# Kernel tuning notes

Measured on AMD Instinct MI355X. Metric: run time of the kernel, lower is better.

## Reference

```python
import jax, jax.numpy as jnp
import numpy as np

L, S, M, N, E, H = 1024, 1024, 256, 8, 512, 8


def embed_rotary(x, cos, sin):
    # x: [B, T, E]; interleaved rotate-half as in RotaryPositionEncoding.embed_rotary
    x2 = jnp.stack([-x[..., 1::2], x[..., 0::2]], axis=-1).reshape(x.shape)
    return x * cos + x2 * sin


def setup_inputs() -> dict:
    key = jax.random.key(0)
    ks = jax.random.split(key, 12)
    return {
        "query": jax.random.normal(ks[0], (L, N, E), jnp.float32),
        "key": jax.random.normal(ks[1], (S, N, E), jnp.float32),
        "value": jax.random.normal(ks[2], (S, N, E), jnp.float32),
        "in_proj_weight": jax.random.normal(ks[3], (3 * E, E), jnp.float32) / np.sqrt(E).astype(np.float32),
        "in_proj_bias": jnp.zeros((3 * E,), jnp.float32),
        "out_proj_weight": jax.random.normal(ks[4], (E, E), jnp.float32) / np.sqrt(E).astype(np.float32),
        "out_proj_bias": jnp.zeros((E,), jnp.float32),
        "rot_q": jax.random.normal(ks[5], (N, L, E, 2), jnp.float32),
        "rot_k": jax.random.normal(ks[6], (N, S, E, 2), jnp.float32),
        "k_mem": jax.random.normal(ks[7], (M, N, E), jnp.float32),
        "v_mem": jax.random.normal(ks[8], (M, N, E), jnp.float32),
        "gate_attn": jax.random.normal(ks[9], (H,), jnp.float32),
        "mem_mask": jax.random.randint(ks[10], (N, M), 0, 2).astype(bool),
        "num_heads": H,
    }


def reference(query, key, value, in_proj_weight, in_proj_bias, out_proj_weight,
              out_proj_bias, rot_q, rot_k, k_mem, v_mem, gate_attn, mem_mask, num_heads):
    L_, N_, E_ = query.shape
    S_ = key.shape[0]
    H_ = num_heads
    hd = E_ // H_
    scale = float(hd) ** -0.5
    # separate q/k/v projections (qkv not identical path)
    q = query @ in_proj_weight[:E_].T + in_proj_bias[:E_]
    k = key @ in_proj_weight[E_:2 * E_].T + in_proj_bias[E_:2 * E_]
    v = value @ in_proj_weight[2 * E_:].T + in_proj_bias[2 * E_:]
    q = q * scale
    # inline rotary PE (applied in batch-first layout, then back)
    q = embed_rotary(q.transpose(1, 0, 2), rot_q[..., 0], rot_q[..., 1]).transpose(1, 0, 2)
    k = embed_rotary(k.transpose(1, 0, 2), rot_k[..., 0], rot_k[..., 1]).transpose(1, 0, 2)
    qh = q.reshape(L_, N_, H_, hd).transpose(1, 2, 0, 3)  # [N,H,L,hd]
    kh = k.reshape(S_, N_, H_, hd).transpose(1, 2, 0, 3)  # [N,H,S,hd]
    vh = v.reshape(S_, N_, H_, hd).transpose(1, 2, 0, 3)
    scores = jnp.einsum('nhld,nhsd->nhls', qh, kh)
    # slot-competition: softmax over queries (slots), then renormalize over keys
    w = jax.nn.softmax(scores, axis=2) + 1e-8
    w = w / w.sum(axis=-1, keepdims=True)
    attn = jnp.einsum('nhls,nhsd->nhld', w, vh)
    # memorizing-transformer style memory K/V branch with sigmoid head gating
    Mm = k_mem.shape[0]
    km = k_mem.reshape(Mm, N_, H_, hd).transpose(1, 2, 0, 3)  # [N,H,M,hd]
    vm = v_mem.reshape(Mm, N_, H_, hd).transpose(1, 2, 0, 3)
    sm = jnp.einsum('nhld,nhmd->nhlm', qh, km)
    sm = jnp.where(mem_mask[:, None, None, :], -1e9, sm)  # additive -inf mask
    wm = jax.nn.softmax(sm, axis=-1)
    om = jnp.einsum('nhlm,nhmd->nhld', wm, vm)
    gate = jax.nn.sigmoid(gate_attn)[None, :, None, None]  # [1,H,1,1]
    attn = gate * om + (1.0 - gate) * attn
    out = attn.transpose(2, 0, 1, 3).reshape(L_, N_, E_)  # back to [L,N,E]
    return out @ out_proj_weight.T + out_proj_bias
```

## Files before the change

### kernel.cpp

```cpp
#include <hip/hip_runtime.h>
#include <hip/hip_bf16.h>

typedef __hip_bfloat16 bf16;
typedef __bf16 bf16x8 __attribute__((ext_vector_type(8)));
typedef float f32x4 __attribute__((ext_vector_type(4)));

#define LQ 1024
#define SK 1024
#define MMEM 256
#define NB 8
#define EE 512
#define NH 8
#define HD 64
#define NBH 64

__device__ inline __bf16 tobf(float f) {
  __hip_bfloat16 h = __float2bfloat16(f);
  return *reinterpret_cast<__bf16*>(&h);
}
__device__ inline float bf2f(__bf16 x) {
  unsigned short u; __builtin_memcpy(&u, &x, 2);
  unsigned int v = (unsigned int)u << 16;
  float f; __builtin_memcpy(&f, &v, 4);
  return f;
}
__device__ inline f32x4 MFMA(bf16x8 a, bf16x8 b, f32x4 c) {
  return __builtin_amdgcn_mfma_f32_16x16x32_bf16(a, b, c, 0, 0, 0);
}

__device__ inline void gload_lds16(const bf16* g, void* l) {
  __builtin_amdgcn_global_load_lds(
      (const __attribute__((address_space(1))) void*)g,
      (__attribute__((address_space(3))) void*)l, 16, 0, 0);
}

__device__ inline bf16x8 load8(const float* p) {
  float4 a = *(const float4*)p;
  float4 b = *(const float4*)(p + 4);
  bf16x8 r;
  r[0] = tobf(a.x); r[1] = tobf(a.y); r[2] = tobf(a.z); r[3] = tobf(a.w);
  r[4] = tobf(b.x); r[5] = tobf(b.y); r[6] = tobf(b.z); r[7] = tobf(b.w);
  return r;
}

#define CVT_T0 524288
#define CVT_T3 98304
#define CVT_T4 32768
__global__ __launch_bounds__(256) void convert5(
    const float* __restrict__ q, const float* __restrict__ k,
    const float* __restrict__ v, const float* __restrict__ w,
    const float* __restrict__ o, bf16* __restrict__ qc, bf16* __restrict__ kc,
    bf16* __restrict__ vc, bf16* __restrict__ wc, bf16* __restrict__ oc)
{
  long long t = (long long)blockIdx.x * 256 + threadIdx.x;
  const float* src; bf16* dst; long long idx;
  if (t < CVT_T0)               { src = q; dst = qc; idx = t; }
  else if (t < 2 * CVT_T0)      { src = k; dst = kc; idx = t - CVT_T0; }
  else if (t < 3 * CVT_T0)      { src = v; dst = vc; idx = t - 2 * CVT_T0; }
  else if (t < 3 * CVT_T0 + CVT_T3) { src = w; dst = wc; idx = t - 3 * CVT_T0; }
  else                          { src = o; dst = oc; idx = t - 3 * CVT_T0 - CVT_T3; }
  *(bf16x8*)(dst + idx * 8) = load8(src + idx * 8);
}

__global__ __launch_bounds__(256) void gemm_proj3(
    const bf16* __restrict__ qc, const bf16* __restrict__ kc,
    const bf16* __restrict__ vc, const bf16* __restrict__ ipwb,
    const float* __restrict__ ipb, bf16* __restrict__ pq,
    bf16* __restrict__ pk, bf16* __restrict__ v_raw)
{
  __shared__ __align__(16) char smem[33792];
  __bf16* As = (__bf16*)smem;
  __bf16* Bs = (__bf16*)(smem + 16384);
  const int z = blockIdx.z;
  const bf16* A = (z == 0) ? qc : (z == 1) ? kc : vc;
  const bf16* W = ipwb + (long long)z * EE * EE;
  const float* bias = ipb + z * EE;
  const float alpha = (z == 0) ? 0.125f : 1.f;
  const int bid2 = blockIdx.y * gridDim.x + blockIdx.x;
  const int xcd = bid2 & 7, sub = bid2 >> 3;
  const int by = (xcd << 3) + (sub >> 2);
  const int bx = sub & 3;
  const int tm0 = by << 7, tn0 = bx << 7;
  const int t = threadIdx.x;
  const int wave = t >> 6, lane = t & 63;
  const int wrow0 = (wave & 1) << 6, wcol0 = (wave >> 1) << 6;
  const int m16 = lane & 15, quad = lane >> 4;

  const f32x4 zero = {0.f, 0.f, 0.f, 0.f};
  f32x4 acc[4][4];
#pragma unroll
  for (int mi = 0; mi < 4; ++mi)
#pragma unroll
    for (int ni = 0; ni < 4; ++ni) acc[mi][ni] = zero;

  const bf16* Ab = A + (long long)tm0 * EE;
  const bf16* Bb = W + (long long)tn0 * EE;
  const int ob_u = wave << 10;

  for (int k0 = 0; k0 < EE; k0 += 64) {
#pragma unroll
    for (int c = 0; c < 4; ++c) {
      int ob = (c << 12) + ob_u;
      int obl = ob + (lane << 4);
      int row = obl >> 7;
      int ce = (obl & 127) >> 1;
      gload_lds16(Ab + (long long)row * EE + k0 + ce, smem + ob);
      gload_lds16(Bb + (long long)row * EE + k0 + ce, smem + 16384 + ob);
    }
    __syncthreads();
#pragma unroll
    for (int kh = 0; kh < 2; ++kh) {
      bf16x8 av[4], bv[4];
#pragma unroll
      for (int i = 0; i < 4; ++i) {
        av[i] = *(bf16x8*)(As + ((wrow0 + (i << 4) + m16) << 6) + (kh << 5) + (quad << 3));
        bv[i] = *(bf16x8*)(Bs + ((wcol0 + (i << 4) + m16) << 6) + (kh << 5) + (quad << 3));
      }
#pragma unroll
      for (int mi = 0; mi < 4; ++mi)
#pragma unroll
        for (int ni = 0; ni < 4; ++ni)
          acc[mi][ni] = MFMA(av[mi], bv[ni], acc[mi][ni]);
    }
    __syncthreads();
  }

  __bf16 (*Cs)[132] = (__bf16(*)[132])smem;
#pragma unroll
  for (int mi = 0; mi < 4; ++mi)
#pragma unroll
    for (int ni = 0; ni < 4; ++ni) {
      int col = wcol0 + (ni << 4) + m16;
      float bv = bias[tn0 + col];
#pragma unroll
      for (int r = 0; r < 4; ++r)
        Cs[wrow0 + (mi << 4) + (quad << 2) + r][col] =
            tobf((acc[mi][ni][r] + bv) * alpha);
    }
  __syncthreads();
  bf16* O = (z == 0) ? pq : (z == 1) ? pk : v_raw;
  const int crow = t >> 1, ch0 = (t & 1) << 6;
  long long gb = (long long)(tm0 + crow) * EE + tn0 + ch0;
#pragma unroll
  for (int j = 0; j < 64; j += 8)
    *(uint4*)(O + gb + j) = *(uint4*)&Cs[crow][ch0 + j];
}

__global__ __launch_bounds__(256) void rotary_kernel(
    const bf16* __restrict__ pq, const bf16* __restrict__ pk,
    const float* __restrict__ rot_q, const float* __restrict__ rot_k,
    bf16* __restrict__ Qh, bf16* __restrict__ Kh)
{
  const bf16* src = blockIdx.y ? pk : pq;
  const float* rot = blockIdx.y ? rot_k : rot_q;
  bf16* dst = blockIdx.y ? Kh : Qh;
  const int t = threadIdx.x;
  const int row = (blockIdx.x << 2) + (t >> 6);
  const int e0 = (t & 63) << 3;
  const int l = row >> 3, n = row & 7;
  bf16x8 x = *(const bf16x8*)(src + (long long)row * EE + e0);
  const float* rp = rot + ((((long long)n * LQ + l) * EE + e0) << 1);
  __bf16 vals[8];
#pragma unroll
  for (int j = 0; j < 8; j += 2) {
    float4 cs4 = *(const float4*)(rp + (j << 1));
    float x0 = bf2f(x[j]);
    float x1 = bf2f(x[j + 1]);
    vals[j]     = tobf(x0 * cs4.x - x1 * cs4.y);
    vals[j + 1] = tobf(x1 * cs4.z + x0 * cs4.w);
  }
  const int h = e0 >> 6, d0 = e0 & 63;
  *(uint4*)(dst + (((long long)(n * NH + h) * LQ + l) * HD + d0)) = *(uint4*)vals;
}

__global__ __launch_bounds__(256) void colsum_kernel(
    const bf16* __restrict__ Qh, const bf16* __restrict__ Kh,
    float* __restrict__ csum)
{
  __shared__ __align__(16) __bf16 Ks[64][72];
  __shared__ __align__(16) __bf16 Qs[64][72];
  __shared__ float cpart[64][2];
  const int bid = blockIdx.y * gridDim.x + blockIdx.x;
  const int xcd = bid & 7, sub = bid >> 3;
  const int b = (xcd << 3) + (sub >> 4);
  const int st0 = (sub & 15) << 6;
  const int t = threadIdx.x;
  const int lrow = t >> 2, lcol = (t & 3) << 4;
  const int wave = t >> 6, lane = t & 63;
  const int wm = (wave & 1) << 5, wn = (wave >> 1) << 5;
  const int m16 = lane & 15, quad = lane >> 4;

  {
    const bf16* kp = Kh + ((long long)b * SK + st0 + lrow) * HD + lcol;
    *(bf16x8*)&Ks[lrow][lcol] = *(const bf16x8*)kp;
    *(bf16x8*)&Ks[lrow][lcol + 8] = *(const bf16x8*)(kp + 8);
  }
  __syncthreads();
  bf16x8 bk[2][2];
#pragma unroll
  for (int ni = 0; ni < 2; ++ni)
#pragma unroll
    for (int kh = 0; kh < 2; ++kh)
      bk[ni][kh] = *(bf16x8*)&Ks[wn + (ni << 4) + m16][(kh << 5) + (quad << 3)];
  __syncthreads();

  const f32x4 zero = {0.f, 0.f, 0.f, 0.f};
  float colp[2] = {0.f, 0.f};
  const bf16* qbase = Qh + ((long long)b * LQ + lrow) * HD + lcol;
  bf16x8 qr0 = *(const bf16x8*)qbase;
  bf16x8 qr1 = *(const bf16x8*)(qbase + 8);
  for (int lt = 0; lt < 16; ++lt) {
    *(bf16x8*)&Qs[lrow][lcol] = qr0;
    *(bf16x8*)&Qs[lrow][lcol + 8] = qr1;
    __syncthreads();
    if (lt < 15) {
      const bf16* qp = qbase + (long long)((lt + 1) << 6) * HD;
      qr0 = *(const bf16x8*)qp;
      qr1 = *(const bf16x8*)(qp + 8);
    }
    f32x4 s00 = zero, s01 = zero, s10 = zero, s11 = zero;
#pragma unroll
    for (int kh = 0; kh < 2; ++kh) {
      bf16x8 a0 = *(bf16x8*)&Qs[wm + m16][(kh << 5) + (quad << 3)];
      bf16x8 a1 = *(bf16x8*)&Qs[wm + 16 + m16][(kh << 5) + (quad << 3)];
      s00 = MFMA(a0, bk[0][kh], s00);
      s01 = MFMA(a0, bk[1][kh], s01);
      s10 = MFMA(a1, bk[0][kh], s10);
      s11 = MFMA(a1, bk[1][kh], s11);
    }
    f32x4 sacc[2][2] = {{s00, s01}, {s10, s11}};
#pragma unroll
    for (int mi = 0; mi < 2; ++mi)
#pragma unroll
      for (int ni = 0; ni < 2; ++ni)
#pragma unroll
        for (int r = 0; r < 4; ++r)
          colp[ni] += __expf(sacc[mi][ni][r]);
    __syncthreads();
  }
  for (int ni = 0; ni < 2; ++ni) {
    float v = colp[ni];
    v += __shfl_down(v, 32, 64);
    v += __shfl_down(v, 16, 64);
    if (quad == 0) cpart[wn + (ni << 4) + m16][wm >> 5] = v;
  }
  __syncthreads();
  if (t < 64) csum[b * SK + st0 + t] = cpart[t][0] + cpart[t][1];
}

__global__ __launch_bounds__(256) void vsum_kernel(
    const bf16* __restrict__ Vt, float* __restrict__ Vsum)
{
  int wid = blockIdx.x * 4 + (threadIdx.x >> 6);
  int lane = threadIdx.x & 63;
  const bf16* p = Vt + (long long)wid * SK + lane * 16;
  float s = 0.f;
  bf16x8 v0 = *(const bf16x8*)p;
  bf16x8 v1 = *(const bf16x8*)(p + 8);
#pragma unroll
  for (int j = 0; j < 8; ++j) s += bf2f(v0[j]) + bf2f(v1[j]);
  for (int off = 32; off; off >>= 1) s += __shfl_down(s, off, 64);
  if (lane == 0) Vsum[wid] = s;
}

__global__ __launch_bounds__(256) void attn_flash(
    const bf16* __restrict__ Qh, const bf16* __restrict__ Kh,
    const bf16* __restrict__ Vt, const float* __restrict__ csum,
    const float* __restrict__ Vsum, bf16* __restrict__ attn)
{
  __shared__ __align__(16) __bf16 Ks[64][72];
  __shared__ __align__(16) __bf16 Vs[64][72];
  __shared__ __align__(16) __bf16 Ps[4096];
  __shared__ __align__(16) float rcs[SK];
  __shared__ float rpart[64][2];
  const int bid = blockIdx.y * gridDim.x + blockIdx.x;
  const int xcd = bid & 7, sub = bid >> 3;
  const int b = (xcd << 3) + (sub >> 4);
  const int tm0 = (sub & 15) << 6;
  const int t = threadIdx.x;
  const int lrow = t >> 2, lcol = (t & 3) << 4;
  const int wave = t >> 6, lane = t & 63;
  const int wm = (wave & 1) << 5, wn = (wave >> 1) << 5;
  const int m16 = lane & 15, quad = lane >> 4;
  const int swz = (m16 & 7) << 4;

#pragma unroll
  for (int i = 0; i < 4; ++i)
    rcs[t + i * 256] = 1.f / csum[b * SK + t + i * 256];
  {
    const bf16* qp = Qh + ((long long)b * LQ + tm0 + lrow) * HD + lcol;
    *(bf16x8*)&Ks[lrow][lcol] = *(const bf16x8*)qp;
    *(bf16x8*)&Ks[lrow][lcol + 8] = *(const bf16x8*)(qp + 8);
  }
  __syncthreads();
  bf16x8 aq[2][2];
#pragma unroll
  for (int li = 0; li < 2; ++li)
#pragma unroll
    for (int kh = 0; kh < 2; ++kh)
      aq[li][kh] = *(bf16x8*)&Ks[wm + (li << 4) + m16][(kh << 5) + (quad << 3)];
  __syncthreads();

  const f32x4 zero = {0.f, 0.f, 0.f, 0.f};
  f32x4 o00 = zero, o01 = zero, o10 = zero, o11 = zero;
  float rsuml[2] = {0.f, 0.f};

  const bf16* kbase = Kh + ((long long)b * SK + lrow) * HD + lcol;
  const bf16* vbase = Vt + ((long long)b * HD + lrow) * SK + lcol;
  bf16x8 kr0 = *(const bf16x8*)kbase;
  bf16x8 kr1 = *(const bf16x8*)(kbase + 8);
  bf16x8 vr0 = *(const bf16x8*)vbase;
  bf16x8 vr1 = *(const bf16x8*)(vbase + 8);

  for (int st = 0; st < 16; ++st) {
    *(bf16x8*)&Ks[lrow][lcol] = kr0;
    *(bf16x8*)&Ks[lrow][lcol + 8] = kr1;
    *(bf16x8*)&Vs[lrow][lcol] = vr0;
    *(bf16x8*)&Vs[lrow][lcol + 8] = vr1;
    __syncthreads();
    if (st < 15) {
      const bf16* kp = kbase + (long long)((st + 1) << 6) * HD;
      const bf16* vp = vbase + ((st + 1) << 6);
      kr0 = *(const bf16x8*)kp;
      kr1 = *(const bf16x8*)(kp + 8);
      vr0 = *(const bf16x8*)vp;
      vr1 = *(const bf16x8*)(vp + 8);
    }
    f32x4 s00 = zero, s01 = zero, s10 = zero, s11 = zero;
#pragma unroll
    for (int kh = 0; kh < 2; ++kh) {
      bf16x8 ak0 = *(bf16x8*)&Ks[wn + m16][(kh << 5) + (quad << 3)];
      bf16x8 ak1 = *(bf16x8*)&Ks[wn + 16 + m16][(kh << 5) + (quad << 3)];
      s00 = MFMA(ak0, aq[0][kh], s00);
      s01 = MFMA(ak0, aq[1][kh], s01);
      s10 = MFMA(ak1, aq[0][kh], s10);
      s11 = MFMA(ak1, aq[1][kh], s11);
    }
    {
      const int lA = wm + m16, lB = wm + 16 + m16;
      char* pA = (char*)Ps + lA * 128;
      char* pB = (char*)Ps + lB * 128;
#pragma unroll
      for (int si = 0; si < 2; ++si) {
        int sloc = wn + (si << 4) + (quad << 2);
        f32x4 rc4 = *(const f32x4*)&rcs[(st << 6) + sloc];
        f32x4 sA = si ? s10 : s00;
        f32x4 sB = si ? s11 : s01;
        __bf16 vA[4], vB[4];
#pragma unroll
        for (int r = 0; r < 4; ++r) {
          float pa = __expf(sA[r]) * rc4[r];
          rsuml[0] += pa; vA[r] = tobf(pa);
          float pb = __expf(sB[r]) * rc4[r];
          rsuml[1] += pb; vB[r] = tobf(pb);
        }
        int sbyte = (sloc << 1) ^ swz;
        *(uint2*)(pA + sbyte) = *(uint2*)vA;
        *(uint2*)(pB + sbyte) = *(uint2*)vB;
      }
    }
    __syncthreads();
#pragma unroll
    for (int kh = 0; kh < 2; ++kh) {
      int sb = (kh << 6) + (quad << 4);
      bf16x8 ap0 = *(bf16x8*)((char*)Ps + (wm + m16) * 128 + (sb ^ swz));
      bf16x8 ap1 = *(bf16x8*)((char*)Ps + (wm + 16 + m16) * 128 + (sb ^ swz));
      bf16x8 bv0 = *(bf16x8*)&Vs[wn + m16][(kh << 5) + (quad << 3)];
      bf16x8 bv1 = *(bf16x8*)&Vs[wn + 16 + m16][(kh << 5) + (quad << 3)];
      o00 = MFMA(ap0, bv0, o00);
      o01 = MFMA(ap0, bv1, o01);
      o10 = MFMA(ap1, bv0, o10);
      o11 = MFMA(ap1, bv1, o11);
    }
    __syncthreads();
  }
#pragma unroll
  for (int li = 0; li < 2; ++li) {
    float v = rsuml[li];
    v += __shfl_xor(v, 16, 64);
    v += __shfl_xor(v, 32, 64);
    if (quad == 0) rpart[wm + (li << 4) + m16][wn >> 5] = v;
  }
  __syncthreads();
  const float* vs = Vsum + b * HD;
  f32x4 oacc[2][2] = {{o00, o01}, {o10, o11}};
  for (int mi = 0; mi < 2; ++mi)
    for (int ni = 0; ni < 2; ++ni) {
      int col = wn + (ni << 4) + m16;
      float vsc = 1e-8f * vs[col];
      for (int r = 0; r < 4; ++r) {
        int row = wm + (mi << 4) + (quad << 2) + r;
        float rs = rpart[row][0] + rpart[row][1];
        Ks[row][col] = tobf((oacc[mi][ni][r] + vsc) / (rs + (float)SK * 1e-8f));
      }
    }
  __syncthreads();
  uint4 u0 = *(uint4*)&Ks[lrow][lcol];
  uint4 u1 = *(uint4*)&Ks[lrow][lcol + 8];
  long long gb = ((long long)b * LQ + tm0 + lrow) * HD + lcol;
  *(uint4*)(attn + gb) = u0;
  *(uint4*)(attn + gb + 8) = u1;
}

__global__ __launch_bounds__(256) void mem_flash(
    const bf16* __restrict__ Qh, const bf16* __restrict__ km,
    const bf16* __restrict__ vmt, const int* __restrict__ mask,
    bf16* __restrict__ omb)
{
  __shared__ __align__(16) __bf16 Ks[64][72];
  __shared__ __align__(16) __bf16 Vs[64][72];
  __shared__ __align__(16) __bf16 Ps[4096];
  __shared__ __align__(16) float mskf[MMEM];
  __shared__ float rpart[64][2];
  const int bid = blockIdx.y * gridDim.x + blockIdx.x;
  const int xcd = bid & 7, sub = bid >> 3;
  const int b = (xcd << 3) + (sub >> 4);
  const int tm0 = (sub & 15) << 6;
  const int n = b >> 3;
  const int t = threadIdx.x;
  const int wave = t >> 6, lane = t & 63;
  const int wm = (wave & 1) << 5, wn = (wave >> 1) << 5;
  const int m16 = lane & 15, quad = lane >> 4;
  const int lrow = t >> 2, lcol = (t & 3) << 4;
  const int swz = (m16 & 7) << 4;

  mskf[t] = mask[n * MMEM + t] ? 0.f : 1.f;
  {
    const bf16* qp = Qh + ((long long)b * LQ + tm0 + lrow) * HD + lcol;
    *(bf16x8*)&Ks[lrow][lcol] = *(const bf16x8*)qp;
    *(bf16x8*)&Ks[lrow][lcol + 8] = *(const bf16x8*)(qp + 8);
  }
  __syncthreads();
  bf16x8 aq[2][2];
#pragma unroll
  for (int li = 0; li < 2; ++li)
#pragma unroll
    for (int kh = 0; kh < 2; ++kh)
      aq[li][kh] = *(bf16x8*)&Ks[wm + (li << 4) + m16][(kh << 5) + (quad << 3)];
  __syncthreads();

  const f32x4 zero = {0.f, 0.f, 0.f, 0.f};
  f32x4 o00 = zero, o01 = zero, o10 = zero, o11 = zero;
  float rsuml[2] = {0.f, 0.f};

  const bf16* kbase = km + ((long long)b * MMEM + lrow) * HD + lcol;
  const bf16* vbase = vmt + ((long long)b * HD + lrow) * MMEM + lcol;
  bf16x8 kr0 = *(const bf16x8*)kbase;
  bf16x8 kr1 = *(const bf16x8*)(kbase + 8);
  bf16x8 vr0 = *(const bf16x8*)vbase;
  bf16x8 vr1 = *(const bf16x8*)(vbase + 8);

  for (int mt = 0; mt < 4; ++mt) {
    *(bf16x8*)&Ks[lrow][lcol] = kr0;
    *(bf16x8*)&Ks[lrow][lcol + 8] = kr1;
    *(bf16x8*)&Vs[lrow][lcol] = vr0;
    *(bf16x8*)&Vs[lrow][lcol + 8] = vr1;
    __syncthreads();
    if (mt < 3) {
      const bf16* kp = kbase + (long long)((mt + 1) << 6) * HD;
      const bf16* vp = vbase + ((mt + 1) << 6);
      kr0 = *(const bf16x8*)kp;
      kr1 = *(const bf16x8*)(kp + 8);
      vr0 = *(const bf16x8*)vp;
      vr1 = *(const bf16x8*)(vp + 8);
    }
    f32x4 s00 = zero, s01 = zero, s10 = zero, s11 = zero;
#pragma unroll
    for (int kh = 0; kh < 2; ++kh) {
      bf16x8 ak0 = *(bf16x8*)&Ks[wn + m16][(kh << 5) + (quad << 3)];
      bf16x8 ak1 = *(bf16x8*)&Ks[wn + 16 + m16][(kh << 5) + (quad << 3)];
      s00 = MFMA(ak0, aq[0][kh], s00);
      s01 = MFMA(ak0, aq[1][kh], s01);
      s10 = MFMA(ak1, aq[0][kh], s10);
      s11 = MFMA(ak1, aq[1][kh], s11);
    }
    {
      const int lA = wm + m16, lB = wm + 16 + m16;
      char* pA = (char*)Ps + lA * 128;
      char* pB = (char*)Ps + lB * 128;
#pragma unroll
      for (int si = 0; si < 2; ++si) {
        int sloc = wn + (si << 4) + (quad << 2);
        f32x4 mf4 = *(const f32x4*)&mskf[(mt << 6) + sloc];
        f32x4 sA = si ? s10 : s00;
        f32x4 sB = si ? s11 : s01;
        __bf16 vA[4], vB[4];
#pragma unroll
        for (int r = 0; r < 4; ++r) {
          float pa = __expf(sA[r]) * mf4[r];
          rsuml[0] += pa; vA[r] = tobf(pa);
          float pb = __expf(sB[r]) * mf4[r];
          rsuml[1] += pb; vB[r] = tobf(pb);
        }
        int sbyte = (sloc << 1) ^ swz;
        *(uint2*)(pA + sbyte) = *(uint2*)vA;
        *(uint2*)(pB + sbyte) = *(uint2*)vB;
      }
    }
    __syncthreads();
#pragma unroll
    for (int kh = 0; kh < 2; ++kh) {
      int sb = (kh << 6) + (quad << 4);
      bf16x8 ap0 = *(bf16x8*)((char*)Ps + (wm + m16) * 128 + (sb ^ swz));
      bf16x8 ap1 = *(bf16x8*)((char*)Ps + (wm + 16 + m16) * 128 + (sb ^ swz));
      bf16x8 bv0 = *(bf16x8*)&Vs[wn + m16][(kh << 5) + (quad << 3)];
      bf16x8 bv1 = *(bf16x8*)&Vs[wn + 16 + m16][(kh << 5) + (quad << 3)];
      o00 = MFMA(ap0, bv0, o00);
      o01 = MFMA(ap0, bv1, o01);
      o10 = MFMA(ap1, bv0, o10);
      o11 = MFMA(ap1, bv1, o11);
    }
    __syncthreads();
  }
#pragma unroll
  for (int li = 0; li < 2; ++li) {
    float v = rsuml[li];
    v += __shfl_xor(v, 16, 64);
    v += __shfl_xor(v, 32, 64);
    if (quad == 0) rpart[wm + (li << 4) + m16][wn >> 5] = v;
  }
  __syncthreads();
  f32x4 oacc[2][2] = {{o00, o01}, {o10, o11}};
  for (int mi = 0; mi < 2; ++mi)
    for (int ni = 0; ni < 2; ++ni) {
      int col = wn + (ni << 4) + m16;
      for (int r = 0; r < 4; ++r) {
        int row = wm + (mi << 4) + (quad << 2) + r;
        float rs = rpart[row][0] + rpart[row][1];
        Ks[row][col] = tobf(oacc[mi][ni][r] / rs);
      }
    }
  __syncthreads();
  uint4 u0 = *(uint4*)&Ks[lrow][lcol];
  uint4 u1 = *(uint4*)&Ks[lrow][lcol + 8];
  long long gb = ((long long)b * LQ + tm0 + lrow) * HD + lcol;
  *(uint4*)(omb + gb) = u0;
  *(uint4*)(omb + gb + 8) = u1;
}

__global__ __launch_bounds__(256) void gemm_out(
    const bf16* __restrict__ attn, const bf16* __restrict__ omb,
    const float* __restrict__ gate, const bf16* __restrict__ opwb,
    const float* __restrict__ opb, float* __restrict__ out)
{
  __shared__ __align__(16) __bf16 As[64][40];
  __shared__ __align__(16) __bf16 Bs[64][40];
  __shared__ float sg[NH];
  const int bid = blockIdx.y * gridDim.x + blockIdx.x;
  const int xcd = bid & 7, sub = bid >> 3;
  const int by = (xcd << 4) + (sub >> 3);
  const int bx = sub & 7;
  const int tm0 = by << 6, tn0 = bx << 6;
  const int t = threadIdx.x;
  const int lrow = t >> 2, lk = (t & 3) << 3;
  const int wave = t >> 6, lane = t & 63;
  const int wm = (wave & 1) << 5, wn = (wave >> 1) << 5;
  const int m16 = lane & 15, quad = lane >> 4;

  if (t < NH) sg[t] = 1.f / (1.f + __expf(-gate[t]));
  __syncthreads();

  const f32x4 zero = {0.f, 0.f, 0.f, 0.f};
  f32x4 acc00 = zero, acc01 = zero, acc10 = zero, acc11 = zero;

  const int row = tm0 + lrow;
  const int l = row >> 3, n = row & 7;
  const bf16* bg = opwb + (long long)(tn0 + lrow) * EE + lk;
  for (int k0 = 0; k0 < EE; k0 += 32) {
    int e = k0 + lk;
    int h = e >> 6, d = e & 63;
    float g = sg[h];
    long long src = (((long long)(n * NH + h) * LQ) + l) * HD + d;
    bf16x8 a8 = *(const bf16x8*)(attn + src);
    bf16x8 o8 = *(const bf16x8*)(omb + src);
    bf16x8 ap;
#pragma unroll
    for (int j = 0; j < 8; ++j)
      ap[j] = tobf(g * bf2f(o8[j]) + (1.f - g) * bf2f(a8[j]));
    *(bf16x8*)&As[lrow][lk] = ap;
    *(bf16x8*)&Bs[lrow][lk] = *(const bf16x8*)(bg + k0);
    __syncthreads();
    bf16x8 a0 = *(bf16x8*)&As[wm + m16][quad << 3];
    bf16x8 a1 = *(bf16x8*)&As[wm + 16 + m16][quad << 3];
    bf16x8 b0 = *(bf16x8*)&Bs[wn + m16][quad << 3];
    bf16x8 b1 = *(bf16x8*)&Bs[wn + 16 + m16][quad << 3];
    acc00 = MFMA(a0, b0, acc00);
    acc01 = MFMA(a0, b1, acc01);
    acc10 = MFMA(a1, b0, acc10);
    acc11 = MFMA(a1, b1, acc11);
    __syncthreads();
  }
  f32x4 accs[2][2] = {{acc00, acc01}, {acc10, acc11}};
  for (int mi = 0; mi < 2; ++mi)
    for (int ni = 0; ni < 2; ++ni) {
      int col = tn0 + wn + (ni << 4) + m16;
      float bv = opb[col];
      long long base = (long long)(tm0 + wm + (mi << 4) + (quad << 2)) * EE + col;
      for (int r = 0; r < 4; ++r)
        out[base + (long long)r * EE] = accs[mi][ni][r] + bv;
    }
}

__global__ __launch_bounds__(256) void v_transpose(
    const bf16* __restrict__ raw, bf16* __restrict__ Vt)
{
  __shared__ __align__(16) __bf16 Ts[64][72];
  const int bh = blockIdx.y;
  const int n = bh >> 3, h = bh & 7;
  const int s0 = blockIdx.x << 6;
  const int t = threadIdx.x;
  const int i = t >> 2, c0 = (t & 3) << 4;
  const bf16* rp = raw + ((long long)(s0 + i) * NB + n) * EE + h * HD + c0;
  *(bf16x8*)&Ts[i][c0] = *(const bf16x8*)rp;
  *(bf16x8*)&Ts[i][c0 + 8] = *(const bf16x8*)(rp + 8);
  __syncthreads();
  const int d = t >> 2, j0 = (t & 3) << 4;
  __bf16 vals[16];
#pragma unroll
  for (int j = 0; j < 16; ++j) vals[j] = Ts[j0 + j][d];
  bf16* wp = Vt + ((long long)bh * HD + d) * SK + s0 + j0;
  *(uint4*)wp = *(uint4*)&vals[0];
  *(uint4*)(wp + 8) = *(uint4*)&vals[8];
}

__global__ __launch_bounds__(256) void mem_prep(
    const float* __restrict__ k_mem, const float* __restrict__ v_mem,
    bf16* __restrict__ km, bf16* __restrict__ vmt)
{
  __shared__ __align__(16) __bf16 Ts[64][72];
  const int bh = blockIdx.y;
  const int n = bh >> 3, h = bh & 7;
  const int m0 = blockIdx.x << 6;
  const int t = threadIdx.x;
  const int i = t >> 2, c0 = (t & 3) << 4;
  const float* kp = k_mem + ((long long)(m0 + i) * NB + n) * EE + h * HD + c0;
  const float* vp = v_mem + ((long long)(m0 + i) * NB + n) * EE + h * HD + c0;
  bf16x8 kv0 = load8(kp), kv1 = load8(kp + 8);
  bf16x8 vv0 = load8(vp), vv1 = load8(vp + 8);
  bf16* kw = km + ((long long)bh * MMEM + m0 + i) * HD + c0;
  *(bf16x8*)kw = kv0;
  *(bf16x8*)(kw + 8) = kv1;
  *(bf16x8*)&Ts[i][c0] = vv0;
  *(bf16x8*)&Ts[i][c0 + 8] = vv1;
  __syncthreads();
  const int d = t >> 2, j0 = (t & 3) << 4;
  __bf16 vals[16];
#pragma unroll
  for (int j = 0; j < 16; ++j) vals[j] = Ts[j0 + j][d];
  bf16* wp = vmt + ((long long)bh * HD + d) * MMEM + m0 + j0;
  *(uint4*)wp = *(uint4*)&vals[0];
  *(uint4*)(wp + 8) = *(uint4*)&vals[8];
}

extern "C" void kernel_launch(void* const* d_in, const int* in_sizes, int n_in,
                              void* d_out, int out_size, void* d_ws, size_t ws_size,
                              hipStream_t stream) {
  const float* query = (const float*)d_in[0];
  const float* key   = (const float*)d_in[1];
  const float* value = (const float*)d_in[2];
  const float* ipw   = (const float*)d_in[3];
  const float* ipb   = (const float*)d_in[4];
  const float* opw   = (const float*)d_in[5];
  const float* opb   = (const float*)d_in[6];
  const float* rot_q = (const float*)d_in[7];
  const float* rot_k = (const float*)d_in[8];
  const float* k_mem = (const float*)d_in[9];
  const float* v_mem = (const float*)d_in[10];
  const float* gate  = (const float*)d_in[11];
  const int*  mask   = (const int*)d_in[12];
  float* out = (float*)d_out;

  char* w = (char*)d_ws;
  size_t off = 0;
  auto carve = [&](size_t bytes) -> char* {
    char* p = w + off;
    off += (bytes + 255) & ~(size_t)255;
    return p;
  };
  bf16* qc    = (bf16*)carve((size_t)LQ * NB * EE * 2);
  bf16* kc    = (bf16*)carve((size_t)SK * NB * EE * 2);
  bf16* vc    = (bf16*)carve((size_t)SK * NB * EE * 2);
  bf16* ipwb  = (bf16*)carve((size_t)3 * EE * EE * 2);
  bf16* opwb  = (bf16*)carve((size_t)EE * EE * 2);
  bf16* v_raw = (bf16*)carve((size_t)SK * NB * EE * 2);
  bf16* Qh    = (bf16*)carve((size_t)NBH * LQ * HD * 2);
  bf16* Kh    = (bf16*)carve((size_t)NBH * SK * HD * 2);
  bf16* Vt    = (bf16*)carve((size_t)NBH * HD * SK * 2);
  bf16* km    = (bf16*)carve((size_t)NBH * MMEM * HD * 2);
  bf16* vmt   = (bf16*)carve((size_t)NBH * HD * MMEM * 2);
  float* csum = (float*)carve((size_t)NBH * SK * 4);
  float* Vsum = (float*)carve((size_t)NBH * HD * 4);
  bf16* attn  = (bf16*)carve((size_t)NBH * LQ * HD * 2);
  bf16* omb   = (bf16*)carve((size_t)NBH * LQ * HD * 2);
  if (off > ws_size) {
    hipMemsetAsync(d_out, 0, (size_t)out_size * 4, stream);
    return;
  }
  bf16* pq = attn;
  bf16* pk = omb;

  convert5<<<(3 * CVT_T0 + CVT_T3 + CVT_T4) / 256, 256, 0, stream>>>(
      query, key, value, ipw, opw, qc, kc, vc, ipwb, opwb);

  gemm_proj3<<<dim3(EE / 128, (LQ * NB) / 128, 3), 256, 0, stream>>>(
      qc, kc, vc, ipwb, ipb, pq, pk, v_raw);

  rotary_kernel<<<dim3((LQ * NB) / 4, 2), 256, 0, stream>>>(
      pq, pk, rot_q, rot_k, Qh, Kh);

  v_transpose<<<dim3(SK / 64, NBH), 256, 0, stream>>>(v_raw, Vt);
  vsum_kernel<<<(NBH * HD) / 4, 256, 0, stream>>>(Vt, Vsum);
  mem_prep<<<dim3(MMEM / 64, NBH), 256, 0, stream>>>(k_mem, v_mem, km, vmt);

  colsum_kernel<<<dim3(SK / 64, NBH), 256, 0, stream>>>(Qh, Kh, csum);

  attn_flash<<<dim3(LQ / 64, NBH), 256, 0, stream>>>(Qh, Kh, Vt, csum, Vsum, attn);
  mem_flash<<<dim3(LQ / 64, NBH), 256, 0, stream>>>(Qh, km, vmt, mask, omb);

  gemm_out<<<dim3(EE / 64, (LQ * NB) / 64, 1), 256, 0, stream>>>(attn, omb, gate, opwb, opb, out);
}
```

Before: 306.0 us.

## Fuse memory-branch attention and gating into main attention kernel; retile output GEMM

Merges the memory K/V softmax branch into the main attention kernel, reusing the loaded Q fragments and applying the sigmoid head gate in the epilogue, so a single combined bf16 tensor is written instead of two. The output projection GEMM is rewritten with 128x128 tiles, 4x4 MFMA accumulators per wave and direct global-to-LDS loads, and no longer blends two inputs. MFMA sections are wrapped in s_setprio hints. This removes one launch, one Q reload and the extra tensor read/write, at the cost of higher register pressure in the fused kernel and fewer GEMM blocks.

Measured after the change: 304.9 us. No clear change (-0.4%).

```diff
diff --git a/kernel.cpp b/kernel.cpp
--- a/kernel.cpp
+++ b/kernel.cpp
@@ -263,20 +263,25 @@
   if (lane == 0) Vsum[wid] = s;
 }
 
-__global__ __launch_bounds__(256) void attn_flash(
+__global__ __launch_bounds__(256) void attn_fused(
     const bf16* __restrict__ Qh, const bf16* __restrict__ Kh,
-    const bf16* __restrict__ Vt, const float* __restrict__ csum,
-    const float* __restrict__ Vsum, bf16* __restrict__ attn)
+    const bf16* __restrict__ Vt, const bf16* __restrict__ km,
+    const bf16* __restrict__ vmt, const float* __restrict__ csum,
+    const float* __restrict__ Vsum, const int* __restrict__ mask,
+    const float* __restrict__ gate, bf16* __restrict__ comb)
 {
   __shared__ __align__(16) __bf16 Ks[64][72];
   __shared__ __align__(16) __bf16 Vs[64][72];
   __shared__ __align__(16) __bf16 Ps[4096];
   __shared__ __align__(16) float rcs[SK];
-  __shared__ float rpart[64][2];
+  __shared__ __align__(16) float mskf[MMEM];
+  __shared__ float rpa[64][2];
+  __shared__ float rpm[64][2];
   const int bid = blockIdx.y * gridDim.x + blockIdx.x;
   const int xcd = bid & 7, sub = bid >> 3;
   const int b = (xcd << 3) + (sub >> 4);
   const int tm0 = (sub & 15) << 6;
+  const int n = b >> 3, h = b & 7;
   const int t = threadIdx.x;
   const int lrow = t >> 2, lcol = (t & 3) << 4;
   const int wave = t >> 6, lane = t & 63;
@@ -287,6 +292,7 @@
 #pragma unroll
   for (int i = 0; i < 4; ++i)
     rcs[t + i * 256] = 1.f / csum[b * SK + t + i * 256];
+  mskf[t] = mask[n * MMEM + t] ? 0.f : 1.f;
   {
     const bf16* qp = Qh + ((long long)b * LQ + tm0 + lrow) * HD + lcol;
     *(bf16x8*)&Ks[lrow][lcol] = *(const bf16x8*)qp;
@@ -302,302 +308,267 @@
   __syncthreads();
 
   const f32x4 zero = {0.f, 0.f, 0.f, 0.f};
+  f32x4 m00 = zero, m01 = zero, m10 = zero, m11 = zero;
+  float rsm[2] = {0.f, 0.f};
+  {
+    const bf16* kbase = km + ((long long)b * MMEM + lrow) * HD + lcol;
+    const bf16* vbase = vmt + ((long long)b * HD + lrow) * MMEM + lcol;
+    bf16x8 kr0 = *(const bf16x8*)kbase;
+    bf16x8 kr1 = *(const bf16x8*)(kbase + 8);
+    bf16x8 vr0 = *(const bf16x8*)vbase;
+    bf16x8 vr1 = *(const bf16x8*)(vbase + 8);
+    for (int mt = 0; mt < 4; ++mt) {
+      *(bf16x8*)&Ks[lrow][lcol] = kr0;
+      *(bf16x8*)&Ks[lrow][lcol + 8] = kr1;
+      *(bf16x8*)&Vs[lrow][lcol] = vr0;
+      *(bf16x8*)&Vs[lrow][lcol + 8] = vr1;
+      __syncthreads();
+      if (mt < 3) {
+        const bf16* kp = kbase + (long long)((mt + 1) << 6) * HD;
+        const bf16* vp = vbase + ((mt + 1) << 6);
+        kr0 = *(const bf16x8*)kp;
+        kr1 = *(const bf16x8*)(kp + 8);
+        vr0 = *(const bf16x8*)vp;
+        vr1 = *(const bf16x8*)(vp + 8);
+      }
+      f32x4 s00 = zero, s01 = zero, s10 = zero, s11 = zero;
+      __builtin_amdgcn_s_setprio(1);
+#pragma unroll
+      for (int kh = 0; kh < 2; ++kh) {
+        bf16x8 ak0 = *(bf16x8*)&Ks[wn + m16][(kh << 5) + (quad << 3)];
+        bf16x8 ak1 = *(bf16x8*)&Ks[wn + 16 + m16][(kh << 5) + (quad << 3)];
+        s00 = MFMA(ak0, aq[0][kh], s00);
+        s01 = MFMA(ak0, aq[1][kh], s01);
+        s10 = MFMA(ak1, aq[0][kh], s10);
+        s11 = MFMA(ak1, aq[1][kh], s11);
+      }
+      __builtin_amdgcn_s_setprio(0);
+      {
+        char* pA = (char*)Ps + (wm + m16) * 128;
+        char* pB = (char*)Ps + (wm + 16 + m16) * 128;
+#pragma unroll
+        for (int si = 0; si < 2; ++si) {
+          int sloc = wn + (si << 4) + (quad << 2);
+          f32x4 mf4 = *(const f32x4*)&mskf[(mt << 6) + sloc];
+          f32x4 sA = si ? s10 : s00;
+          f32x4 sB = si ? s11 : s01;
+          __bf16 vA[4], vB[4];
+#pragma unroll
+          for (int r = 0; r < 4; ++r) {
+            float pa = __expf(sA[r]) * mf4[r];
+            rsm[0] += pa; vA[r] = tobf(pa);
+            float pb = __expf(sB[r]) * mf4[r];
+            rsm[1] += pb; vB[r] = tobf(pb);
+          }
+          int sbyte = (sloc << 1) ^ swz;
+          *(uint2*)(pA + sbyte) = *(uint2*)vA;
+          *(uint2*)(pB + sbyte) = *(uint2*)vB;
+        }
+      }
+      __syncthreads();
+      __builtin_amdgcn_s_setprio(1);
+#pragma unroll
+      for (int kh = 0; kh < 2; ++kh) {
+        int sb = (kh << 6) + (quad << 4);
+        bf16x8 ap0 = *(bf16x8*)((char*)Ps + (wm + m16) * 128 + (sb ^ swz));
+        bf16x8 ap1 = *(bf16x8*)((char*)Ps + (wm + 16 + m16) * 128 + (sb ^ swz));
+        bf16x8 bv0 = *(bf16x8*)&Vs[wn + m16][(kh << 5) + (quad << 3)];
+        bf16x8 bv1 = *(bf16x8*)&Vs[wn + 16 + m16][(kh << 5) + (quad << 3)];
+        m00 = MFMA(ap0, bv0, m00);
+        m01 = MFMA(ap0, bv1, m01);
+        m10 = MFMA(ap1, bv0, m10);
+        m11 = MFMA(ap1, bv1, m11);
+      }
+      __builtin_amdgcn_s_setprio(0);
+      __syncthreads();
+    }
+  }
+
   f32x4 o00 = zero, o01 = zero, o10 = zero, o11 = zero;
-  float rsuml[2] = {0.f, 0.f};
-
-  const bf16* kbase = Kh + ((long long)b * SK + lrow) * HD + lcol;
-  const bf16* vbase = Vt + ((long long)b * HD + lrow) * SK + lcol;
-  bf16x8 kr0 = *(const bf16x8*)kbase;
-  bf16x8 kr1 = *(const bf16x8*)(kbase + 8);
-  bf16x8 vr0 = *(const bf16x8*)vbase;
-  bf16x8 vr1 = *(const bf16x8*)(vbase + 8);
-
-  for (int st = 0; st < 16; ++st) {
-    *(bf16x8*)&Ks[lrow][lcol] = kr0;
-    *(bf16x8*)&Ks[lrow][lcol + 8] = kr1;
-    *(bf16x8*)&Vs[lrow][lcol] = vr0;
-    *(bf16x8*)&Vs[lrow][lcol + 8] = vr1;
-    __syncthreads();
-    if (st < 15) {
-      const bf16* kp = kbase + (long long)((st + 1) << 6) * HD;
-      const bf16* vp = vbase + ((st + 1) << 6);
-      kr0 = *(const bf16x8*)kp;
-      kr1 = *(const bf16x8*)(kp + 8);
-      vr0 = *(const bf16x8*)vp;
-      vr1 = *(const bf16x8*)(vp + 8);
-    }
-    f32x4 s00 = zero, s01 = zero, s10 = zero, s11 = zero;
-#pragma unroll
-    for (int kh = 0; kh < 2; ++kh) {
-      bf16x8 ak0 = *(bf16x8*)&Ks[wn + m16][(kh << 5) + (quad << 3)];
-      bf16x8 ak1 = *(bf16x8*)&Ks[wn + 16 + m16][(kh << 5) + (quad << 3)];
-      s00 = MFMA(ak0, aq[0][kh], s00);
-      s01 = MFMA(ak0, aq[1][kh], s01);
-      s10 = MFMA(ak1, aq[0][kh], s10);
-      s11 = MFMA(ak1, aq[1][kh], s11);
-    }
-    {
-      const int lA = wm + m16, lB = wm + 16 + m16;
-      char* pA = (char*)Ps + lA * 128;
-      char* pB = (char*)Ps + lB * 128;
-#pragma unroll
-      for (int si = 0; si < 2; ++si) {
-        int sloc = wn + (si << 4) + (quad << 2);
-        f32x4 rc4 = *(const f32x4*)&rcs[(st << 6) + sloc];
-        f32x4 sA = si ? s10 : s00;
-        f32x4 sB = si ? s11 : s01;
-        __bf16 vA[4], vB[4];
-#pragma unroll
-        for (int r = 0; r < 4; ++r) {
-          float pa = __expf(sA[r]) * rc4[r];
-          rsuml[0] += pa; vA[r] = tobf(pa);
-          float pb = __expf(sB[r]) * rc4[r];
-          rsuml[1] += pb; vB[r] = tobf(pb);
+  float rsa[2] = {0.f, 0.f};
+  {
+    const bf16* kbase = Kh + ((long long)b * SK + lrow) * HD + lcol;
+    const bf16* vbase = Vt + ((long long)b * HD + lrow) * SK + lcol;
+    bf16x8 kr0 = *(const bf16x8*)kbase;
+    bf16x8 kr1 = *(const bf16x8*)(kbase + 8);
+    bf16x8 vr0 = *(const bf16x8*)vbase;
+    bf16x8 vr1 = *(const bf16x8*)(vbase + 8);
+    for (int st = 0; st < 16; ++st) {
+      *(bf16x8*)&Ks[lrow][lcol] = kr0;
+      *(bf16x8*)&Ks[lrow][lcol + 8] = kr1;
+      *(bf16x8*)&Vs[lrow][lcol] = vr0;
+      *(bf16x8*)&Vs[lrow][lcol + 8] = vr1;
+      __syncthreads();
+      if (st < 15) {
+        const bf16* kp = kbase + (long long)((st + 1) << 6) * HD;
+        const bf16* vp = vbase + ((st + 1) << 6);
+        kr0 = *(const bf16x8*)kp;
+        kr1 = *(const bf16x8*)(kp + 8);
+        vr0 = *(const bf16x8*)vp;
+        vr1 = *(const bf16x8*)(vp + 8);
+      }
+      f32x4 s00 = zero, s01 = zero, s10 = zero, s11 = zero;
+      __builtin_amdgcn_s_setprio(1);
+#pragma unroll
+      for (int kh = 0; kh < 2; ++kh) {
+        bf16x8 ak0 = *(bf16x8*)&Ks[wn + m16][(kh << 5) + (quad << 3)];
+        bf16x8 ak1 = *(bf16x8*)&Ks[wn + 16 + m16][(kh << 5) + (quad << 3)];
+        s00 = MFMA(ak0, aq[0][kh], s00);
+        s01 = MFMA(ak0, aq[1][kh], s01);
+        s10 = MFMA(ak1, aq[0][kh], s10);
+        s11 = MFMA(ak1, aq[1][kh], s11);
+      }
+      __builtin_amdgcn_s_setprio(0);
+      {
+        char* pA = (char*)Ps + (wm + m16) * 128;
+        char* pB = (char*)Ps + (wm + 16 + m16) * 128;
+#pragma unroll
+        for (int si = 0; si < 2; ++si) {
+          int sloc = wn + (si << 4) + (quad << 2);
+          f32x4 rc4 = *(const f32x4*)&rcs[(st << 6) + sloc];
+          f32x4 sA = si ? s10 : s00;
+          f32x4 sB = si ? s11 : s01;
+          __bf16 vA[4], vB[4];
+#pragma unroll
+          for (int r = 0; r < 4; ++r) {
+            float pa = __expf(sA[r]) * rc4[r];
+            rsa[0] += pa; vA[r] = tobf(pa);
+            float pb = __expf(sB[r]) * rc4[r];
+            rsa[1] += pb; vB[r] = tobf(pb);
+          }
+          int sbyte = (sloc << 1) ^ swz;
+          *(uint2*)(pA + sbyte) = *(uint2*)vA;
+          *(uint2*)(pB + sbyte) = *(uint2*)vB;
         }
-        int sbyte = (sloc << 1) ^ swz;
-        *(uint2*)(pA + sbyte) = *(uint2*)vA;
-        *(uint2*)(pB + sbyte) = *(uint2*)vB;
-      }
-    }
-    __syncthreads();
-#pragma unroll
-    for (int kh = 0; kh < 2; ++kh) {
-      int sb = (kh << 6) + (quad << 4);
-      bf16x8 ap0 = *(bf16x8*)((char*)Ps + (wm + m16) * 128 + (sb ^ swz));
-      bf16x8 ap1 = *(bf16x8*)((char*)Ps + (wm + 16 + m16) * 128 + (sb ^ swz));
-      bf16x8 bv0 = *(bf16x8*)&Vs[wn + m16][(kh << 5) + (quad << 3)];
-      bf16x8 bv1 = *(bf16x8*)&Vs[wn + 16 + m16][(kh << 5) + (quad << 3)];
-      o00 = MFMA(ap0, bv0, o00);
-      o01 = MFMA(ap0, bv1, o01);
-      o10 = MFMA(ap1, bv0, o10);
-      o11 = MFMA(ap1, bv1, o11);
-    }
-    __syncthreads();
-  }
+      }
+      __syncthreads();
+      __builtin_amdgcn_s_setprio(1);
+#pragma unroll
+      for (int kh = 0; kh < 2; ++kh) {
+        int sb = (kh << 6) + (quad << 4);
+        bf16x8 ap0 = *(bf16x8*)((char*)Ps + (wm + m16) * 128 + (sb ^ swz));
+        bf16x8 ap1 = *(bf16x8*)((char*)Ps + (wm + 16 + m16) * 128 + (sb ^ swz));
+        bf16x8 bv0 = *(bf16x8*)&Vs[wn + m16][(kh << 5) + (quad << 3)];
+        bf16x8 bv1 = *(bf16x8*)&Vs[wn + 16 + m16][(kh << 5) + (quad << 3)];
+        o00 = MFMA(ap0, bv0, o00);
+        o01 = MFMA(ap0, bv1, o01);
+        o10 = MFMA(ap1, bv0, o10);
+        o11 = MFMA(ap1, bv1, o11);
+      }
+      __builtin_amdgcn_s_setprio(0);
+      __syncthreads();
+    }
+  }
+
 #pragma unroll
   for (int li = 0; li < 2; ++li) {
-    float v = rsuml[li];
-    v += __shfl_xor(v, 16, 64);
-    v += __shfl_xor(v, 32, 64);
-    if (quad == 0) rpart[wm + (li << 4) + m16][wn >> 5] = v;
-  }
-  __syncthreads();
+    float va = rsa[li];
+    va += __shfl_xor(va, 16, 64);
+    va += __shfl_xor(va, 32, 64);
+    float vm = rsm[li];
+    vm += __shfl_xor(vm, 16, 64);
+    vm += __shfl_xor(vm, 32, 64);
+    if (quad == 0) {
+      rpa[wm + (li << 4) + m16][wn >> 5] = va;
+      rpm[wm + (li << 4) + m16][wn >> 5] = vm;
+    }
+  }
+  __syncthreads();
+
   const float* vs = Vsum + b * HD;
+  const float g = 1.f / (1.f + __expf(-gate[h]));
   f32x4 oacc[2][2] = {{o00, o01}, {o10, o11}};
+  f32x4 macc[2][2] = {{m00, m01}, {m10, m11}};
   for (int mi = 0; mi < 2; ++mi)
     for (int ni = 0; ni < 2; ++ni) {
       int col = wn + (ni << 4) + m16;
       float vsc = 1e-8f * vs[col];
       for (int r = 0; r < 4; ++r) {
         int row = wm + (mi << 4) + (quad << 2) + r;
-        float rs = rpart[row][0] + rpart[row][1];
-        Ks[row][col] = tobf((oacc[mi][ni][r] + vsc) / (rs + (float)SK * 1e-8f));
+        float ra = rpa[row][0] + rpa[row][1];
+        float rm = rpm[row][0] + rpm[row][1];
+        float oa = (oacc[mi][ni][r] + vsc) / (ra + (float)SK * 1e-8f);
+        float om = macc[mi][ni][r] / rm;
+        Ks[row][col] = tobf(g * om + (1.f - g) * oa);
       }
     }
   __syncthreads();
   uint4 u0 = *(uint4*)&Ks[lrow][lcol];
   uint4 u1 = *(uint4*)&Ks[lrow][lcol + 8];
   long long gb = ((long long)b * LQ + tm0 + lrow) * HD + lcol;
-  *(uint4*)(attn + gb) = u0;
-  *(uint4*)(attn + gb + 8) = u1;
-}
-
-__global__ __launch_bounds__(256) void mem_flash(
-    const bf16* __restrict__ Qh, const bf16* __restrict__ km,
-    const bf16* __restrict__ vmt, const int* __restrict__ mask,
-    bf16* __restrict__ omb)
-{
-  __shared__ __align__(16) __bf16 Ks[64][72];
-  __shared__ __align__(16) __bf16 Vs[64][72];
-  __shared__ __align__(16) __bf16 Ps[4096];
-  __shared__ __align__(16) float mskf[MMEM];
-  __shared__ float rpart[64][2];
-  const int bid = blockIdx.y * gridDim.x + blockIdx.x;
-  const int xcd = bid & 7, sub = bid >> 3;
-  const int b = (xcd << 3) + (sub >> 4);
-  const int tm0 = (sub & 15) << 6;
-  const int n = b >> 3;
+  *(uint4*)(comb + gb) = u0;
+  *(uint4*)(comb + gb + 8) = u1;
+}
+
+__global__ __launch_bounds__(256) void gemm_out(
+    const bf16* __restrict__ comb, const bf16* __restrict__ opwb,
+    const float* __restrict__ opb, float* __restrict__ out)
+{
+  __shared__ __align__(16) char smem[32768];
+  __bf16* As = (__bf16*)smem;
+  __bf16* Bs = (__bf16*)(smem + 16384);
+  const int bid2 = blockIdx.y * gridDim.x + blockIdx.x;
+  const int xcd = bid2 & 7, sub = bid2 >> 3;
+  const int by = (xcd << 3) + (sub >> 2);
+  const int bx = sub & 3;
+  const int tm0 = by << 7, tn0 = bx << 7;
   const int t = threadIdx.x;
   const int wave = t >> 6, lane = t & 63;
-  const int wm = (wave & 1) << 5, wn = (wave >> 1) << 5;
+  const int wrow0 = (wave & 1) << 6, wcol0 = (wave >> 1) << 6;
   const int m16 = lane & 15, quad = lane >> 4;
-  const int lrow = t >> 2, lcol = (t & 3) << 4;
-  const int swz = (m16 & 7) << 4;
-
-  mskf[t] = mask[n * MMEM + t] ? 0.f : 1.f;
-  {
-    const bf16* qp = Qh + ((long long)b * LQ + tm0 + lrow) * HD + lcol;
-    *(bf16x8*)&Ks[lrow][lcol] = *(const bf16x8*)qp;
-    *(bf16x8*)&Ks[lrow][lcol + 8] = *(const bf16x8*)(qp + 8);
-  }
-  __syncthreads();
-  bf16x8 aq[2][2];
-#pragma unroll
-  for (int li = 0; li < 2; ++li)
-#pragma unroll
-    for (int kh = 0; kh < 2; ++kh)
-      aq[li][kh] = *(bf16x8*)&Ks[wm + (li << 4) + m16][(kh << 5) + (quad << 3)];
-  __syncthreads();
 
   const f32x4 zero = {0.f, 0.f, 0.f, 0.f};
-  f32x4 o00 = zero, o01 = zero, o10 = zero, o11 = zero;
-  float rsuml[2] = {0.f, 0.f};
-
-  const bf16* kbase = km + ((long long)b * MMEM + lrow) * HD + lcol;
-  const bf16* vbase = vmt + ((long long)b * HD + lrow) * MMEM + lcol;
-  bf16x8 kr0 = *(const bf16x8*)kbase;
-  bf16x8 kr1 = *(const bf16x8*)(kbase + 8);
-  bf16x8 vr0 = *(const bf16x8*)vbase;
-  bf16x8 vr1 = *(const bf16x8*)(vbase + 8);
-
-  for (int mt = 0; mt < 4; ++mt) {
-    *(bf16x8*)&Ks[lrow][lcol] = kr0;
-    *(bf16x8*)&Ks[lrow][lcol + 8] = kr1;
-    *(bf16x8*)&Vs[lrow][lcol] = vr0;
-    *(bf16x8*)&Vs[lrow][lcol + 8] = vr1;
+  f32x4 acc[4][4];
+#pragma unroll
+  for (int mi = 0; mi < 4; ++mi)
+#pragma unroll
+    for (int ni = 0; ni < 4; ++ni) acc[mi][ni] = zero;
+
+  const bf16* Bb = opwb + (long long)tn0 * EE;
+  const int ob_u = wave << 10;
+
+  for (int k0 = 0; k0 < EE; k0 += 64) {
+    const int h = k0 >> 6;
+#pragma unroll
+    for (int c = 0; c < 4; ++c) {
+      int ob = (c << 12) + ob_u;
+      int obl = ob + (lane << 4);
+      int row = obl >> 7;
+      int ce = (obl & 127) >> 1;
+      int arow = tm0 + row;
+      int l = arow >> 3, nn = arow & 7;
+      gload_lds16(comb + (((long long)(nn * NH + h) * LQ + l) * HD + ce),
+                  smem + ob);
+      gload_lds16(Bb + (long long)row * EE + k0 + ce, smem + 16384 + ob);
+    }
     __syncthreads();
-    if (mt < 3) {
-      const bf16* kp = kbase + (long long)((mt + 1) << 6) * HD;
-      const bf16* vp = vbase + ((mt + 1) << 6);
-      kr0 = *(const bf16x8*)kp;
-      kr1 = *(const bf16x8*)(kp + 8);
-      vr0 = *(const bf16x8*)vp;
-      vr1 = *(const bf16x8*)(vp + 8);
-    }
-    f32x4 s00 = zero, s01 = zero, s10 = zero, s11 = zero;
 #pragma unroll
     for (int kh = 0; kh < 2; ++kh) {
-      bf16x8 ak0 = *(bf16x8*)&Ks[wn + m16][(kh << 5) + (quad << 3)];
-      bf16x8 ak1 = *(bf16x8*)&Ks[wn + 16 + m16][(kh << 5) + (quad << 3)];
-      s00 = MFMA(ak0, aq[0][kh], s00);
-      s01 = MFMA(ak0, aq[1][kh], s01);
-      s10 = MFMA(ak1, aq[0][kh], s10);
-      s11 = MFMA(ak1, aq[1][kh], s11);
-    }
-    {
-      const int lA = wm + m16, lB = wm + 16 + m16;
-      char* pA = (char*)Ps + lA * 128;
-      char* pB = (char*)Ps + lB * 128;
-#pragma unroll
-      for (int si = 0; si < 2; ++si) {
-        int sloc = wn + (si << 4) + (quad << 2);
-        f32x4 mf4 = *(const f32x4*)&mskf[(mt << 6) + sloc];
-        f32x4 sA = si ? s10 : s00;
-        f32x4 sB = si ? s11 : s01;
-        __bf16 vA[4], vB[4];
-#pragma unroll
-        for (int r = 0; r < 4; ++r) {
-          float pa = __expf(sA[r]) * mf4[r];
-          rsuml[0] += pa; vA[r] = tobf(pa);
-          float pb = __expf(sB[r]) * mf4[r];
-          rsuml[1] += pb; vB[r] = tobf(pb);
-        }
-        int sbyte = (sloc << 1) ^ swz;
-        *(uint2*)(pA + sbyte) = *(uint2*)vA;
-        *(uint2*)(pB + sbyte) = *(uint2*)vB;
-      }
+      bf16x8 av[4], bv[4];
+#pragma unroll
+      for (int i = 0; i < 4; ++i) {
+        av[i] = *(bf16x8*)(As + ((wrow0 + (i << 4) + m16) << 6) + (kh << 5) + (quad << 3));
+        bv[i] = *(bf16x8*)(Bs + ((wcol0 + (i << 4) + m16) << 6) + (kh << 5) + (quad << 3));
+      }
+#pragma unroll
+      for (int mi = 0; mi < 4; ++mi)
+#pragma unroll
+        for (int ni = 0; ni < 4; ++ni)
+          acc[mi][ni] = MFMA(av[mi], bv[ni], acc[mi][ni]);
     }
     __syncthreads();
-#pragma unroll
-    for (int kh = 0; kh < 2; ++kh) {
-      int sb = (kh << 6) + (quad << 4);
-      bf16x8 ap0 = *(bf16x8*)((char*)Ps + (wm + m16) * 128 + (sb ^ swz));
-      bf16x8 ap1 = *(bf16x8*)((char*)Ps + (wm + 16 + m16) * 128 + (sb ^ swz));
-      bf16x8 bv0 = *(bf16x8*)&Vs[wn + m16][(kh << 5) + (quad << 3)];
-      bf16x8 bv1 = *(bf16x8*)&Vs[wn + 16 + m16][(kh << 5) + (quad << 3)];
-      o00 = MFMA(ap0, bv0, o00);
-      o01 = MFMA(ap0, bv1, o01);
-      o10 = MFMA(ap1, bv0, o10);
-      o11 = MFMA(ap1, bv1, o11);
-    }
-    __syncthreads();
-  }
-#pragma unroll
-  for (int li = 0; li < 2; ++li) {
-    float v = rsuml[li];
-    v += __shfl_xor(v, 16, 64);
-    v += __shfl_xor(v, 32, 64);
-    if (quad == 0) rpart[wm + (li << 4) + m16][wn >> 5] = v;
-  }
-  __syncthreads();
-  f32x4 oacc[2][2] = {{o00, o01}, {o10, o11}};
-  for (int mi = 0; mi < 2; ++mi)
-    for (int ni = 0; ni < 2; ++ni) {
-      int col = wn + (ni << 4) + m16;
-      for (int r = 0; r < 4; ++r) {
-        int row = wm + (mi << 4) + (quad << 2) + r;
-        float rs = rpart[row][0] + rpart[row][1];
-        Ks[row][col] = tobf(oacc[mi][ni][r] / rs);
-      }
-    }
-  __syncthreads();
-  uint4 u0 = *(uint4*)&Ks[lrow][lcol];
-  uint4 u1 = *(uint4*)&Ks[lrow][lcol + 8];
-  long long gb = ((long long)b * LQ + tm0 + lrow) * HD + lcol;
-  *(uint4*)(omb + gb) = u0;
-  *(uint4*)(omb + gb + 8) = u1;
-}
-
-__global__ __launch_bounds__(256) void gemm_out(
-    const bf16* __restrict__ attn, const bf16* __restrict__ omb,
-    const float* __restrict__ gate, const bf16* __restrict__ opwb,
-    const float* __restrict__ opb, float* __restrict__ out)
-{
-  __shared__ __align__(16) __bf16 As[64][40];
-  __shared__ __align__(16) __bf16 Bs[64][40];
-  __shared__ float sg[NH];
-  const int bid = blockIdx.y * gridDim.x + blockIdx.x;
-  const int xcd = bid & 7, sub = bid >> 3;
-  const int by = (xcd << 4) + (sub >> 3);
-  const int bx = sub & 7;
-  const int tm0 = by << 6, tn0 = bx << 6;
-  const int t = threadIdx.x;
-  const int lrow = t >> 2, lk = (t & 3) << 3;
-  const int wave = t >> 6, lane = t & 63;
-  const int wm = (wave & 1) << 5, wn = (wave >> 1) << 5;
-  const int m16 = lane & 15, quad = lane >> 4;
-
-  if (t < NH) sg[t] = 1.f / (1.f + __expf(-gate[t]));
-  __syncthreads();
-
-  const f32x4 zero = {0.f, 0.f, 0.f, 0.f};
-  f32x4 acc00 = zero, acc01 = zero, acc10 = zero, acc11 = zero;
-
-  const int row = tm0 + lrow;
-  const int l = row >> 3, n = row & 7;
-  const bf16* bg = opwb + (long long)(tn0 + lrow) * EE + lk;
-  for (int k0 = 0; k0 < EE; k0 += 32) {
-    int e = k0 + lk;
-    int h = e >> 6, d = e & 63;
-    float g = sg[h];
-    long long src = (((long long)(n * NH + h) * LQ) + l) * HD + d;
-    bf16x8 a8 = *(const bf16x8*)(attn + src);
-    bf16x8 o8 = *(const bf16x8*)(omb + src);
-    bf16x8 ap;
-#pragma unroll
-    for (int j = 0; j < 8; ++j)
-      ap[j] = tobf(g * bf2f(o8[j]) + (1.f - g) * bf2f(a8[j]));
-    *(bf16x8*)&As[lrow][lk] = ap;
-    *(bf16x8*)&Bs[lrow][lk] = *(const bf16x8*)(bg + k0);
-    __syncthreads();
-    bf16x8 a0 = *(bf16x8*)&As[wm + m16][quad << 3];
-    bf16x8 a1 = *(bf16x8*)&As[wm + 16 + m16][quad << 3];
-    bf16x8 b0 = *(bf16x8*)&Bs[wn + m16][quad << 3];
-    bf16x8 b1 = *(bf16x8*)&Bs[wn + 16 + m16][quad << 3];
-    acc00 = MFMA(a0, b0, acc00);
-    acc01 = MFMA(a0, b1, acc01);
-    acc10 = MFMA(a1, b0, acc10);
-    acc11 = MFMA(a1, b1, acc11);
-    __syncthreads();
-  }
-  f32x4 accs[2][2] = {{acc00, acc01}, {acc10, acc11}};
-  for (int mi = 0; mi < 2; ++mi)
-    for (int ni = 0; ni < 2; ++ni) {
-      int col = tn0 + wn + (ni << 4) + m16;
+  }
+
+#pragma unroll
+  for (int mi = 0; mi < 4; ++mi)
+#pragma unroll
+    for (int ni = 0; ni < 4; ++ni) {
+      int col = tn0 + wcol0 + (ni << 4) + m16;
       float bv = opb[col];
-      long long base = (long long)(tm0 + wm + (mi << 4) + (quad << 2)) * EE + col;
+      int row0 = tm0 + wrow0 + (mi << 4) + (quad << 2);
+#pragma unroll
       for (int r = 0; r < 4; ++r)
-        out[base + (long long)r * EE] = accs[mi][ni][r] + bv;
+        out[(long long)(row0 + r) * EE + col] = acc[mi][ni][r] + bv;
     }
 }
 
@@ -690,14 +661,14 @@
   bf16* vmt   = (bf16*)carve((size_t)NBH * HD * MMEM * 2);
   float* csum = (float*)carve((size_t)NBH * SK * 4);
   float* Vsum = (float*)carve((size_t)NBH * HD * 4);
-  bf16* attn  = (bf16*)carve((size_t)NBH * LQ * HD * 2);
-  bf16* omb   = (bf16*)carve((size_t)NBH * LQ * HD * 2);
+  bf16* comb  = (bf16*)carve((size_t)NBH * LQ * HD * 2);
+  bf16* pkbuf = (bf16*)carve((size_t)NBH * LQ * HD * 2);
   if (off > ws_size) {
     hipMemsetAsync(d_out, 0, (size_t)out_size * 4, stream);
     return;
   }
-  bf16* pq = attn;
-  bf16* pk = omb;
+  bf16* pq = comb;
+  bf16* pk = pkbuf;
 
   convert5<<<(3 * CVT_T0 + CVT_T3 + CVT_T4) / 256, 256, 0, stream>>>(
       query, key, value, ipw, opw, qc, kc, vc, ipwb, opwb);
@@ -714,8 +685,8 @@
 
   colsum_kernel<<<dim3(SK / 64, NBH), 256, 0, stream>>>(Qh, Kh, csum);
 
-  attn_flash<<<dim3(LQ / 64, NBH), 256, 0, stream>>>(Qh, Kh, Vt, csum, Vsum, attn);
-  mem_flash<<<dim3(LQ / 64, NBH), 256, 0, stream>>>(Qh, km, vmt, mask, omb);
-
-  gemm_out<<<dim3(EE / 64, (LQ * NB) / 64, 1), 256, 0, stream>>>(attn, omb, gate, opwb, opb, out);
-}
+  attn_fused<<<dim3(LQ / 64, NBH), 256, 0, stream>>>(
+      Qh, Kh, Vt, km, vmt, csum, Vsum, mask, gate, comb);
+
+  gemm_out<<<dim3(4, 64), 256, 0, stream>>>(comb, opwb, opb, out);
+}
```
